# Kernel optimization log

Hardware: AMD Instinct MI355X
Metric: run time of the kernel (lower is better)

## Reference

```python
import jax, jax.numpy as jnp
import numpy as np

ALPHA = 0.2  # LeakyReLU negative slope (args.alpha)

def _leaky(x):
    return jnp.where(x >= 0, x, ALPHA * x)

def setup_inputs() -> dict:
    key = jax.random.key(0)
    k1, k2, k3, k4 = jax.random.split(key, 4)
    B, N, F_in, F_out = 4, 2048, 512, 512
    h = jax.random.normal(k1, (B, N, F_in), dtype=jnp.float32)
    W = jax.random.normal(k2, (F_in, F_out), dtype=jnp.float32) * 0.05
    a = jax.random.normal(k3, (2 * F_out, 1), dtype=jnp.float32) * 0.05
    adj = jax.random.randint(k4, (B, N, N), 0, 2, dtype=jnp.int32)
    return {"h": h, "W": W, "a": a, "adj": adj}

def reference(h, W, a, adj):
    F_out = W.shape[1]
    Wh = jnp.matmul(h, W)                      # [B, N, F_out]
    # a_input is built under torch.no_grad() in the original -> stop_gradient
    Wh_sg = jax.lax.stop_gradient(Wh)
    a1 = a[:F_out, 0]                          # score for node i (repeat_interleave side)
    a2 = a[F_out:, 0]                          # score for node j (repeat side)
    s_i = Wh_sg @ a1                           # [B, N]
    s_j = Wh_sg @ a2                           # [B, N]
    e = _leaky(s_i[:, :, None] + s_j[:, None, :])   # [B, N, N]
    e = jnp.where(adj > 0, e, jnp.float32(-9e15))
    attention = jax.nn.softmax(e, axis=1)      # softmax over dim=1, as in original
    # dropout skipped (eval mode, training=False)
    h_prime = jnp.einsum('bij,bjf->bif', attention, Wh)
    return _leaky(h_prime)                     # concat=True
```

## Files before the change

### kernel.cpp

```cpp
#include <hip/hip_runtime.h>

#define BB 4
#define NN 2048
#define FF 512
#define ALPHA 0.2f

typedef unsigned short u16;
typedef unsigned int u32;
typedef __attribute__((ext_vector_type(8))) short bf16x8;
typedef __attribute__((ext_vector_type(4))) float f32x4;

__device__ __forceinline__ u16 f2bf(float x) {
  union { float f; u32 u; } v; v.f = x;
  u32 r = v.u + 0x7fffu + ((v.u >> 16) & 1u);
  return (u16)(r >> 16);
}
__device__ __forceinline__ float leaky(float x) { return x >= 0.f ? x : ALPHA * x; }

__global__ __launch_bounds__(256) void k_wa(const float* __restrict__ W,
                                            const float* __restrict__ a,
                                            float* __restrict__ wa1,
                                            float* __restrict__ wa2) {
  const int wave = threadIdx.x >> 6, lane = threadIdx.x & 63;
  const int k = blockIdx.x * 4 + wave;
  const int f0 = lane * 8;
  float4 w0 = *(const float4*)(W + (size_t)k * FF + f0);
  float4 w1 = *(const float4*)(W + (size_t)k * FF + f0 + 4);
  float4 p0 = *(const float4*)(a + f0);
  float4 p1 = *(const float4*)(a + f0 + 4);
  float4 q0 = *(const float4*)(a + FF + f0);
  float4 q1 = *(const float4*)(a + FF + f0 + 4);
  float d1 = w0.x*p0.x + w0.y*p0.y + w0.z*p0.z + w0.w*p0.w
           + w1.x*p1.x + w1.y*p1.y + w1.z*p1.z + w1.w*p1.w;
  float d2 = w0.x*q0.x + w0.y*q0.y + w0.z*q0.z + w0.w*q0.w
           + w1.x*q1.x + w1.y*q1.y + w1.z*q1.z + w1.w*q1.w;
#pragma unroll
  for (int o = 32; o; o >>= 1) { d1 += __shfl_xor(d1, o); d2 += __shfl_xor(d2, o); }
  if (lane == 0) { wa1[k] = d1; wa2[k] = d2; }
}

__global__ __launch_bounds__(256) void k_wt(const float* __restrict__ W,
                                            u16* __restrict__ wt) {
  __shared__ float T[64][65];
  const int k0 = blockIdx.x * 64, f0 = blockIdx.y * 64;
  const int tid = threadIdx.x;
  const int c = tid & 15, r0 = tid >> 4;
#pragma unroll
  for (int p = 0; p < 4; p++) {
    const int k = r0 + p * 16;
    float4 v = *(const float4*)(W + (size_t)(k0 + k) * FF + f0 + c * 4);
    T[c * 4 + 0][k] = v.x;
    T[c * 4 + 1][k] = v.y;
    T[c * 4 + 2][k] = v.z;
    T[c * 4 + 3][k] = v.w;
  }
  __syncthreads();
  const int kc = tid & 7, fr0 = tid >> 3;
#pragma unroll
  for (int p = 0; p < 2; p++) {
    const int f = fr0 + p * 32;
    union { uint4 q; u16 s[8]; } o;
#pragma unroll
    for (int q = 0; q < 8; q++) o.s[q] = f2bf(T[f][kc * 8 + q]);
    *(uint4*)(wt + (size_t)(f0 + f) * FF + k0 + kc * 8) = o.q;
  }
}

__global__ __launch_bounds__(256) void k_s(const float* __restrict__ h,
                                           const float* __restrict__ wa1,
                                           const float* __restrict__ wa2,
                                           float* __restrict__ s1,
                                           float* __restrict__ s2,
                                           u16* __restrict__ hbf) {
  const int wave = threadIdx.x >> 6, lane = threadIdx.x & 63;
  const int row = blockIdx.x * 4 + wave;
  const int f0 = lane * 8;
  float4 h0 = *(const float4*)(h + (size_t)row * FF + f0);
  float4 h1 = *(const float4*)(h + (size_t)row * FF + f0 + 4);
  float4 p0 = *(const float4*)(wa1 + f0);
  float4 p1 = *(const float4*)(wa1 + f0 + 4);
  float4 q0 = *(const float4*)(wa2 + f0);
  float4 q1 = *(const float4*)(wa2 + f0 + 4);
  union { uint4 q; u16 s[8]; } ob;
  ob.s[0] = f2bf(h0.x); ob.s[1] = f2bf(h0.y); ob.s[2] = f2bf(h0.z); ob.s[3] = f2bf(h0.w);
  ob.s[4] = f2bf(h1.x); ob.s[5] = f2bf(h1.y); ob.s[6] = f2bf(h1.z); ob.s[7] = f2bf(h1.w);
  *(uint4*)(hbf + (size_t)row * FF + f0) = ob.q;
  float d1 = h0.x*p0.x + h0.y*p0.y + h0.z*p0.z + h0.w*p0.w
           + h1.x*p1.x + h1.y*p1.y + h1.z*p1.z + h1.w*p1.w;
  float d2 = h0.x*q0.x + h0.y*q0.y + h0.z*q0.z + h0.w*q0.w
           + h1.x*q1.x + h1.y*q1.y + h1.z*q1.z + h1.w*q1.w;
#pragma unroll
  for (int o = 32; o; o >>= 1) { d1 += __shfl_xor(d1, o); d2 += __shfl_xor(d2, o); }
  if (lane == 0) { s1[row] = d1; s2[row] = d2; }
}

__global__ __launch_bounds__(512) void k_l(const int* __restrict__ adj,
                                           const float* __restrict__ s1,
                                           const float* __restrict__ s2,
                                           float* __restrict__ lpart,
                                           u16* __restrict__ P) {
  const int b = blockIdx.y, t = threadIdx.x;
  const int rh = t >> 8;
  const int tj = t & 255, j8 = tj * 8;
  const int i0 = blockIdx.x * 16 + rh * 8;
  float s2v[8];
  *(float4*)(&s2v[0]) = *(const float4*)(s2 + b * NN + j8);
  *(float4*)(&s2v[4]) = *(const float4*)(s2 + b * NN + j8 + 4);
  float accv[8];
#pragma unroll
  for (int k = 0; k < 8; k++) accv[k] = 0.f;
  const int* abase = adj + ((size_t)b * NN + i0) * NN + j8;
  u16* pbase = P + ((size_t)b * NN + i0) * NN + j8;
#pragma unroll 4
  for (int i = 0; i < 8; i++) {
    int4 A0 = *(const int4*)(abase + (size_t)i * NN);
    int4 A1 = *(const int4*)(abase + (size_t)i * NN + 4);
    const float s1i = s1[b * NN + i0 + i];
    int av[8] = {A0.x, A0.y, A0.z, A0.w, A1.x, A1.y, A1.z, A1.w};
    union { uint4 q; u16 s[8]; } o;
#pragma unroll
    for (int k = 0; k < 8; k++) {
      float p = (av[k] > 0) ? __expf(leaky(s1i + s2v[k])) : 0.f;
      accv[k] += p;
      o.s[k] = f2bf(p);
    }
    *(uint4*)(pbase + (size_t)i * NN) = o.q;
  }
  float* lp = lpart + (size_t)(blockIdx.x * 2 + rh) * (BB * NN) + b * NN + j8;
  *(float4*)lp = *(float4*)(&accv[0]);
  *(float4*)(lp + 4) = *(float4*)(&accv[4]);
}

__global__ __launch_bounds__(256) void k_lred(const float* __restrict__ lpart,
                                              float* __restrict__ l) {
  const int idx = blockIdx.x * 256 + threadIdx.x;
  float s = 0.f;
#pragma unroll 8
  for (int c = 0; c < 256; c++) s += lpart[(size_t)c * (BB * NN) + idx];
  l[idx] = s;
}

__global__ __launch_bounds__(256) void k_wh(const u16* __restrict__ hbf,
                                            const u16* __restrict__ wt,
                                            const float* __restrict__ l,
                                            u16* __restrict__ whT) {
  __shared__ __attribute__((aligned(16))) u16 As[2][64][64];
  __shared__ __attribute__((aligned(16))) u16 Bs[2][64][64];
  const int bid = blockIdx.x;
  const int L = (bid & 7) * 128 + (bid >> 3);
  const int it = L >> 3, ft = L & 7;
  const int iG0 = it * 64;
  const int b = iG0 >> 11, icol0 = iG0 & (NN - 1);
  const int f0 = ft * 64;
  const int tid = threadIdx.x, wave = tid >> 6, lane = tid & 63;
  const int wm = (wave >> 1) * 32, wn = (wave & 1) * 32;

  const int srow = lane >> 3;
  const int scol = (((lane & 7) ^ (srow & 7)) << 3);
  const u16* gA0 = wt + ((size_t)(f0 + wave * 16 + srow)) * FF + scol;
  const u16* gB0 = hbf + ((size_t)(iG0 + wave * 16 + srow)) * FF + scol;

  f32x4 acc[2][2];
#pragma unroll
  for (int x = 0; x < 2; x++)
#pragma unroll
    for (int y = 0; y < 2; y++) acc[x][y] = f32x4{0.f, 0.f, 0.f, 0.f};

  auto STAGE = [&](int buf, int off16) {
#pragma unroll
    for (int p = 0; p < 2; p++)
      __builtin_amdgcn_global_load_lds(
          (const __attribute__((address_space(1))) void*)(gA0 + (size_t)p * 8 * FF + off16),
          (__attribute__((address_space(3))) void*)(&As[buf][wave * 16 + p * 8][0]), 16, 0, 0);
#pragma unroll
    for (int p = 0; p < 2; p++)
      __builtin_amdgcn_global_load_lds(
          (const __attribute__((address_space(1))) void*)(gB0 + (size_t)p * 8 * FF + off16),
          (__attribute__((address_space(3))) void*)(&Bs[buf][wave * 16 + p * 8][0]), 16, 0, 0);
  };

  STAGE(0, 0);

  int cur = 0;
  const int r = lane & 15, kq = lane >> 4;
  const int sx = (r & 7) << 3;
  for (int t = 0; t < 8; t++) {
    if (t < 7) {
      STAGE(cur ^ 1, (t + 1) * 64);
      asm volatile("s_waitcnt vmcnt(4)" ::: "memory");
    } else {
      asm volatile("s_waitcnt vmcnt(0)" ::: "memory");
    }
    __builtin_amdgcn_s_barrier();
#pragma unroll
    for (int kk = 0; kk < 2; kk++) {
      bf16x8 af[2], bv[2];
#pragma unroll
      for (int mi = 0; mi < 2; mi++)
        af[mi] = *(const bf16x8*)(&As[cur][wm + mi * 16 + r][(kk * 32 + kq * 8) ^ sx]);
#pragma unroll
      for (int ni = 0; ni < 2; ni++)
        bv[ni] = *(const bf16x8*)(&Bs[cur][wn + ni * 16 + r][(kk * 32 + kq * 8) ^ sx]);
#pragma unroll
      for (int mi = 0; mi < 2; mi++)
#pragma unroll
        for (int ni = 0; ni < 2; ni++)
          acc[mi][ni] = __builtin_amdgcn_mfma_f32_16x16x32_bf16(af[mi], bv[ni], acc[mi][ni], 0, 0, 0);
    }
    __builtin_amdgcn_s_barrier();
    cur ^= 1;
  }

  const int rg = lane >> 4;
#pragma unroll
  for (int ni = 0; ni < 2; ni++) {
    const int icol = icol0 + wn + ni * 16 + r;
    const float rl = __builtin_amdgcn_rcpf(l[b * NN + icol]);
#pragma unroll
    for (int mi = 0; mi < 2; mi++) {
#pragma unroll
      for (int rr = 0; rr < 4; rr++) {
        const int f = f0 + wm + mi * 16 + rg * 4 + rr;
        whT[((size_t)b * FF + f) * NN + icol] = f2bf(acc[mi][ni][rr] * rl);
      }
    }
  }
}

__global__ __launch_bounds__(512) void k_out(const u16* __restrict__ P,
                                             const u16* __restrict__ whS,
                                             float* __restrict__ out) {
  __shared__ __attribute__((aligned(16))) u16 As[2][128][64];
  __shared__ __attribute__((aligned(16))) u16 Bs[2][64][64];
  const int bid = blockIdx.x;
  const int L = (bid & 7) * 64 + (bid >> 3);
  const int b = L >> 7, it = (L >> 3) & 15, ft = L & 7;
  const int i0 = it * 128, f0 = ft * 64;
  const int tid = threadIdx.x, wave = tid >> 6, lane = tid & 63;
  const int wm = (wave >> 1) * 32, wn = (wave & 1) * 32;

  const int srow = lane >> 3;
  const int scol = (((lane & 7) ^ (srow & 7)) << 3);
  const u16* gA0 = P + ((size_t)(b * NN + i0 + wave * 16 + srow)) * NN + scol;
  const u16* gB0 = whS + ((size_t)(b * FF + f0 + wave * 8 + srow)) * NN + scol;

  f32x4 acc[2][2];
#pragma unroll
  for (int x = 0; x < 2; x++)
#pragma unroll
    for (int y = 0; y < 2; y++) acc[x][y] = f32x4{0.f, 0.f, 0.f, 0.f};

  auto STAGE = [&](int buf, int off16) {
#pragma unroll
    for (int p = 0; p < 2; p++)
      __builtin_amdgcn_global_load_lds(
          (const __attribute__((address_space(1))) void*)(gA0 + (size_t)p * 8 * NN + off16),
          (__attribute__((address_space(3))) void*)(&As[buf][wave * 16 + p * 8][0]), 16, 0, 0);
    __builtin_amdgcn_global_load_lds(
        (const __attribute__((address_space(1))) void*)(gB0 + off16),
        (__attribute__((address_space(3))) void*)(&Bs[buf][wave * 8][0]), 16, 0, 0);
  };

  STAGE(0, 0);

  int cur = 0;
  const int r = lane & 15, kq = lane >> 4;
  const int sx = (r & 7) << 3;
  for (int t = 0; t < 32; t++) {
    if (t < 31) {
      STAGE(cur ^ 1, (t + 1) * 64);
      asm volatile("s_waitcnt vmcnt(3)" ::: "memory");
    } else {
      asm volatile("s_waitcnt vmcnt(0)" ::: "memory");
    }
    __builtin_amdgcn_s_barrier();
#pragma unroll
    for (int kk = 0; kk < 2; kk++) {
      bf16x8 af[2], bv[2];
#pragma unroll
      for (int mi = 0; mi < 2; mi++)
        af[mi] = *(const bf16x8*)(&As[cur][wm + mi * 16 + r][(kk * 32 + kq * 8) ^ sx]);
#pragma unroll
      for (int ni = 0; ni < 2; ni++)
        bv[ni] = *(const bf16x8*)(&Bs[cur][wn + ni * 16 + r][(kk * 32 + kq * 8) ^ sx]);
#pragma unroll
      for (int mi = 0; mi < 2; mi++)
#pragma unroll
        for (int ni = 0; ni < 2; ni++)
          acc[mi][ni] = __builtin_amdgcn_mfma_f32_16x16x32_bf16(af[mi], bv[ni], acc[mi][ni], 0, 0, 0);
    }
    __builtin_amdgcn_s_barrier();
    cur ^= 1;
  }

  const int rg = lane >> 4;
#pragma unroll
  for (int mi = 0; mi < 2; mi++)
#pragma unroll
    for (int ni = 0; ni < 2; ni++) {
      const int f = f0 + wn + ni * 16 + r;
#pragma unroll
      for (int rr = 0; rr < 4; rr++) {
        const int i = i0 + wm + mi * 16 + rg * 4 + rr;
        out[((size_t)b * NN + i) * FF + f] = leaky(acc[mi][ni][rr]);
      }
    }
}

extern "C" void kernel_launch(void* const* d_in, const int* in_sizes, int n_in,
                              void* d_out, int out_size, void* d_ws, size_t ws_size,
                              hipStream_t stream) {
  const float* h = (const float*)d_in[0];
  const float* W = (const float*)d_in[1];
  const float* a = (const float*)d_in[2];
  const int* adj = (const int*)d_in[3];
  float* out = (float*)d_out;

  char* ws = (char*)d_ws;
  u16* whT = (u16*)ws;
  float* lpart = (float*)ws;
  u16* P = (u16*)(ws + (size_t)8388608);
  float* s1 = (float*)(ws + (size_t)8388608 + 33554432);
  float* s2 = s1 + BB * NN;
  float* lsum = s2 + BB * NN;
  float* wa1 = lsum + BB * NN;
  float* wa2 = wa1 + FF;
  u16* hbf = (u16*)(wa2 + FF);
  u16* wt = hbf + (size_t)BB * NN * FF;

  k_wa<<<dim3(128), 256, 0, stream>>>(W, a, wa1, wa2);
  k_wt<<<dim3(8, 8), 256, 0, stream>>>(W, wt);
  k_s<<<dim3(2048), 256, 0, stream>>>(h, wa1, wa2, s1, s2, hbf);
  k_l<<<dim3(128, 4), 512, 0, stream>>>(adj, s1, s2, lpart, P);
  k_lred<<<dim3(32), 256, 0, stream>>>(lpart, lsum);
  k_wh<<<dim3(1024), 256, 0, stream>>>(hbf, wt, lsum, whT);
  k_out<<<dim3(512), 512, 0, stream>>>(P, whT, out);
}
```

Baseline: 82.76 us.

## Merge W prep kernels, parallelize l reduction, triple-buffer k_out pipeline

```diff
diff --git a/kernel.cpp b/kernel.cpp
--- a/kernel.cpp
+++ b/kernel.cpp
@@ -17,52 +17,52 @@
 }
 __device__ __forceinline__ float leaky(float x) { return x >= 0.f ? x : ALPHA * x; }
 
-__global__ __launch_bounds__(256) void k_wa(const float* __restrict__ W,
-                                            const float* __restrict__ a,
-                                            float* __restrict__ wa1,
-                                            float* __restrict__ wa2) {
-  const int wave = threadIdx.x >> 6, lane = threadIdx.x & 63;
-  const int k = blockIdx.x * 4 + wave;
-  const int f0 = lane * 8;
-  float4 w0 = *(const float4*)(W + (size_t)k * FF + f0);
-  float4 w1 = *(const float4*)(W + (size_t)k * FF + f0 + 4);
-  float4 p0 = *(const float4*)(a + f0);
-  float4 p1 = *(const float4*)(a + f0 + 4);
-  float4 q0 = *(const float4*)(a + FF + f0);
-  float4 q1 = *(const float4*)(a + FF + f0 + 4);
-  float d1 = w0.x*p0.x + w0.y*p0.y + w0.z*p0.z + w0.w*p0.w
-           + w1.x*p1.x + w1.y*p1.y + w1.z*p1.z + w1.w*p1.w;
-  float d2 = w0.x*q0.x + w0.y*q0.y + w0.z*q0.z + w0.w*q0.w
-           + w1.x*q1.x + w1.y*q1.y + w1.z*q1.z + w1.w*q1.w;
-#pragma unroll
-  for (int o = 32; o; o >>= 1) { d1 += __shfl_xor(d1, o); d2 += __shfl_xor(d2, o); }
-  if (lane == 0) { wa1[k] = d1; wa2[k] = d2; }
-}
-
-__global__ __launch_bounds__(256) void k_wt(const float* __restrict__ W,
-                                            u16* __restrict__ wt) {
+__global__ __launch_bounds__(256) void k_wawt(const float* __restrict__ W,
+                                              const float* __restrict__ a,
+                                              float* __restrict__ wa1,
+                                              float* __restrict__ wa2,
+                                              u16* __restrict__ wt) {
   __shared__ float T[64][65];
-  const int k0 = blockIdx.x * 64, f0 = blockIdx.y * 64;
   const int tid = threadIdx.x;
-  const int c = tid & 15, r0 = tid >> 4;
-#pragma unroll
-  for (int p = 0; p < 4; p++) {
-    const int k = r0 + p * 16;
-    float4 v = *(const float4*)(W + (size_t)(k0 + k) * FF + f0 + c * 4);
-    T[c * 4 + 0][k] = v.x;
-    T[c * 4 + 1][k] = v.y;
-    T[c * 4 + 2][k] = v.z;
-    T[c * 4 + 3][k] = v.w;
-  }
-  __syncthreads();
-  const int kc = tid & 7, fr0 = tid >> 3;
-#pragma unroll
-  for (int p = 0; p < 2; p++) {
-    const int f = fr0 + p * 32;
-    union { uint4 q; u16 s[8]; } o;
-#pragma unroll
-    for (int q = 0; q < 8; q++) o.s[q] = f2bf(T[f][kc * 8 + q]);
-    *(uint4*)(wt + (size_t)(f0 + f) * FF + k0 + kc * 8) = o.q;
+  if (blockIdx.x < 64) {
+    const int k0 = (blockIdx.x & 7) * 64, f0 = (blockIdx.x >> 3) * 64;
+    const int c = tid & 15, r0 = tid >> 4;
+#pragma unroll
+    for (int p = 0; p < 4; p++) {
+      const int k = r0 + p * 16;
+      float4 v = *(const float4*)(W + (size_t)(k0 + k) * FF + f0 + c * 4);
+      T[c * 4 + 0][k] = v.x;
+      T[c * 4 + 1][k] = v.y;
+      T[c * 4 + 2][k] = v.z;
+      T[c * 4 + 3][k] = v.w;
+    }
+    __syncthreads();
+    const int kc = tid & 7, fr0 = tid >> 3;
+#pragma unroll
+    for (int p = 0; p < 2; p++) {
+      const int f = fr0 + p * 32;
+      union { uint4 q; u16 s[8]; } o;
+#pragma unroll
+      for (int q = 0; q < 8; q++) o.s[q] = f2bf(T[f][kc * 8 + q]);
+      *(uint4*)(wt + (size_t)(f0 + f) * FF + k0 + kc * 8) = o.q;
+    }
+  } else {
+    const int wave = tid >> 6, lane = tid & 63;
+    const int k = (blockIdx.x - 64) * 4 + wave;
+    const int f0 = lane * 8;
+    float4 w0 = *(const float4*)(W + (size_t)k * FF + f0);
+    float4 w1 = *(const float4*)(W + (size_t)k * FF + f0 + 4);
+    float4 p0 = *(const float4*)(a + f0);
+    float4 p1 = *(const float4*)(a + f0 + 4);
+    float4 q0 = *(const float4*)(a + FF + f0);
+    float4 q1 = *(const float4*)(a + FF + f0 + 4);
+    float d1 = w0.x*p0.x + w0.y*p0.y + w0.z*p0.z + w0.w*p0.w
+             + w1.x*p1.x + w1.y*p1.y + w1.z*p1.z + w1.w*p1.w;
+    float d2 = w0.x*q0.x + w0.y*q0.y + w0.z*q0.z + w0.w*q0.w
+             + w1.x*q1.x + w1.y*q1.y + w1.z*q1.z + w1.w*q1.w;
+#pragma unroll
+    for (int o = 32; o; o >>= 1) { d1 += __shfl_xor(d1, o); d2 += __shfl_xor(d2, o); }
+    if (lane == 0) { wa1[k] = d1; wa2[k] = d2; }
   }
 }
 
@@ -133,11 +133,21 @@
 
 __global__ __launch_bounds__(256) void k_lred(const float* __restrict__ lpart,
                                               float* __restrict__ l) {
-  const int idx = blockIdx.x * 256 + threadIdx.x;
+  __shared__ float red[8][32];
+  const int t = threadIdx.x;
+  const int io = t & 31, cg = t >> 5;
+  const int idx = blockIdx.x * 32 + io;
   float s = 0.f;
 #pragma unroll 8
-  for (int c = 0; c < 256; c++) s += lpart[(size_t)c * (BB * NN) + idx];
-  l[idx] = s;
+  for (int c = cg; c < 256; c += 8) s += lpart[(size_t)c * (BB * NN) + idx];
+  red[cg][io] = s;
+  __syncthreads();
+  if (t < 32) {
+    float r = 0.f;
+#pragma unroll
+    for (int g = 0; g < 8; g++) r += red[g][t];
+    l[blockIdx.x * 32 + t] = r;
+  }
 }
 
 __global__ __launch_bounds__(256) void k_wh(const u16* __restrict__ hbf,
@@ -230,8 +240,8 @@
 __global__ __launch_bounds__(512) void k_out(const u16* __restrict__ P,
                                              const u16* __restrict__ whS,
                                              float* __restrict__ out) {
-  __shared__ __attribute__((aligned(16))) u16 As[2][128][64];
-  __shared__ __attribute__((aligned(16))) u16 Bs[2][64][64];
+  __shared__ __attribute__((aligned(16))) u16 As[3][128][64];
+  __shared__ __attribute__((aligned(16))) u16 Bs[3][64][64];
   const int bid = blockIdx.x;
   const int L = (bid & 7) * 64 + (bid >> 3);
   const int b = L >> 7, it = (L >> 3) & 15, ft = L & 7;
@@ -262,13 +272,17 @@
   };
 
   STAGE(0, 0);
+  STAGE(1, 64);
 
   int cur = 0;
   const int r = lane & 15, kq = lane >> 4;
   const int sx = (r & 7) << 3;
   for (int t = 0; t < 32; t++) {
-    if (t < 31) {
-      STAGE(cur ^ 1, (t + 1) * 64);
+    if (t <= 29) {
+      int nb = cur - 1; if (nb < 0) nb += 3;
+      STAGE(nb, (t + 2) * 64);
+      asm volatile("s_waitcnt vmcnt(6)" ::: "memory");
+    } else if (t == 30) {
       asm volatile("s_waitcnt vmcnt(3)" ::: "memory");
     } else {
       asm volatile("s_waitcnt vmcnt(0)" ::: "memory");
@@ -290,7 +304,7 @@
           acc[mi][ni] = __builtin_amdgcn_mfma_f32_16x16x32_bf16(af[mi], bv[ni], acc[mi][ni], 0, 0, 0);
     }
     __builtin_amdgcn_s_barrier();
-    cur ^= 1;
+    cur = (cur == 2) ? 0 : cur + 1;
   }
 
   const int rg = lane >> 4;
@@ -328,11 +342,10 @@
   u16* hbf = (u16*)(wa2 + FF);
   u16* wt = hbf + (size_t)BB * NN * FF;
 
-  k_wa<<<dim3(128), 256, 0, stream>>>(W, a, wa1, wa2);
-  k_wt<<<dim3(8, 8), 256, 0, stream>>>(W, wt);
+  k_wawt<<<dim3(192), 256, 0, stream>>>(W, a, wa1, wa2, wt);
   k_s<<<dim3(2048), 256, 0, stream>>>(h, wa1, wa2, s1, s2, hbf);
   k_l<<<dim3(128, 4), 512, 0, stream>>>(adj, s1, s2, lpart, P);
-  k_lred<<<dim3(32), 256, 0, stream>>>(lpart, lsum);
+  k_lred<<<dim3(256), 256, 0, stream>>>(lpart, lsum);
   k_wh<<<dim3(1024), 256, 0, stream>>>(hbf, wt, lsum, whT);
   k_out<<<dim3(512), 512, 0, stream>>>(P, whT, out);
 }
```

Measured after the change: 73.87 us (median of 2 runs). 10.7% less time.
